# Kernel tuning notes

Hardware: AMD Instinct MI355X
Metric: run time of the kernel (lower is better)

Reference implementation:

```python
import jax, jax.numpy as jnp
import numpy as np

NH = 8        # num_heads
HD = 6        # head_dim
DIM = NH * HD # 48
KS = 3        # kernel_size
NT = KS ** 3  # 27 neighborhood tokens
SCALE = HD ** -0.5


def setup_inputs() -> dict:
    key = jax.random.key(0)
    k1, k2, k3 = jax.random.split(key, 3)
    B, H, W, T = 1, 40, 40, 40
    q = jax.random.normal(k1, (B, H, W, T, DIM), jnp.float32)
    k = jax.random.normal(k2, (B, H, W, T, DIM), jnp.float32)
    # learned relative position bias (torch init is zeros; use small noise so it matters)
    rpb = jax.random.normal(k3, (NH, KS, KS, KS), jnp.float32) * 0.02
    return {"q": q, "k": k, "rpb": rpb}


def _neighborhood_attention(q, k, rpb):
    B, H, W, T, C = q.shape
    # pad keys by win_size=1 on each spatial side (zero pad, as in nnf.pad)
    kp = jnp.pad(k, ((0, 0), (1, 1), (1, 1), (1, 1), (0, 0)))
    # gather the 27 shifted views -> [B,H,W,T,27,C] (equivalent of unfold+permute)
    win = jnp.stack(
        [kp[:, i:i + H, j:j + W, l:l + T, :]
         for i in range(KS) for j in range(KS) for l in range(KS)],
        axis=4,
    )
    qh = q.reshape(B, H, W, T, NH, HD) * SCALE          # [B,H,W,T,nh,hd]
    kh = win.reshape(B, H, W, T, NT, NH, HD)            # [B,H,W,T,27,nh,hd]
    attn = jnp.einsum('bxyzhd,bxyzkhd->bxyzhk', qh, kh)
    attn = attn + rpb.reshape(NH, NT)[None, None, None, None]  # rel-pos bias
    attn = jax.nn.softmax(attn, axis=-1)                # [B,H,W,T,nh,27]
    # value = constant integer offsets of the 3x3x3 window (makeV)
    r = jnp.arange(-(KS // 2), KS // 2 + 1, dtype=q.dtype)
    offs = jnp.stack(jnp.meshgrid(r, r, r, indexing='ij'), axis=-1).reshape(NT, 3)
    out = jnp.einsum('bxyzhk,ko->bxyzho', attn, offs)   # [B,H,W,T,nh,3]
    return out.reshape(B, H, W, T, NH * 3).transpose(0, 4, 1, 2, 3)


def reference(q, k, rpb):
    return _neighborhood_attention(q, k, rpb)
```

## Files before the change

### kernel.cpp

```cpp
#include <hip/hip_runtime.h>


#define GS   40
#define NVOX (GS*GS*GS)
#define VST  36

typedef __fp16 half2_t __attribute__((ext_vector_type(2)));
typedef float  f2      __attribute__((ext_vector_type(2)));

__device__ __forceinline__ float fdot2(half2_t a, half2_t b, float c) {
    return __builtin_amdgcn_fdot2(a, b, c, false);
}
__device__ __forceinline__ half2_t h2(unsigned int u) {
    return __builtin_bit_cast(half2_t, u);
}
__device__ __forceinline__ unsigned int pk(float a, float b) {
    return __builtin_bit_cast(unsigned int, __builtin_amdgcn_cvt_pkrtz(a, b));
}

__global__ __launch_bounds__(512, 4) void natt_kernel(
    const float* __restrict__ q, const float* __restrict__ kk,
    const float* __restrict__ rpb, float* __restrict__ out)
{
    __shared__ __align__(16) unsigned int sk[360 * VST];
    __shared__ float srpb[4 * 72];

    int t = threadIdx.x;
    int b = blockIdx.x;
    int xcd = b & 7, off = b >> 3;
    int w = (xcd < 4 ? xcd * 63 : 252 + (xcd - 4) * 62) + off;
    int bz = w % 5, byx = w / 5;
    int by = byx % 10, bx = byx / 10;
    int x0 = bx * 4, y0 = by * 4, z0 = bz * 8;

    int hp = t & 3;
    int v  = t >> 2;
    int vz = v & 7, vy = (v >> 3) & 3, vx = v >> 5;
    int gvox = (x0 + vx) * 1600 + (y0 + vy) * 40 + (z0 + vz);
    const float4* qp = (const float4*)q + (size_t)gvox * 12 + hp * 3;
    float4 qa = qp[0], qb = qp[1], qc = qp[2];

    if (t < 216) {
        int h = t / 27, n = t - h * 27;
        int i = n / 9, r9 = n - i * 9;
        int j = r9 / 3, l = r9 - j * 3;
        srpb[(h >> 1) * 72 + ((i * 3 + j) * 4 + l) * 2 + (h & 1)] =
            rpb[t] * 1.4426950408889634f;
    }

    if (t < 360) {
        int hx = t / 60, r60 = t - hx * 60;
        int hy = r60 / 10, hz = r60 - hy * 10;
        int gx = x0 + hx - 1, gy = y0 + hy - 1, gz = z0 + hz - 1;
        unsigned m = (((unsigned)gx < GS) & ((unsigned)gy < GS) &
                      ((unsigned)gz < GS)) ? 0xffffffffu : 0u;
        int cx = min(max(gx, 0), GS - 1);
        int cy = min(max(gy, 0), GS - 1);
        int cz = min(max(gz, 0), GS - 1);
        const float4* src = (const float4*)kk +
                            (size_t)(cx * 1600 + cy * 40 + cz) * 12;
        unsigned int* dst = sk + t * VST;
        #pragma unroll
        for (int hpc = 0; hpc < 4; ++hpc) {
            float4 f0 = src[hpc * 3 + 0];
            float4 f1 = src[hpc * 3 + 1];
            float4 fv = src[hpc * 3 + 2];
            uint4 u4v;
            u4v.x = pk(f0.x, f0.y) & m; u4v.y = pk(f0.z, f0.w) & m;
            u4v.z = pk(f1.x, f1.y) & m; u4v.w = pk(f1.z, f1.w) & m;
            uint2 u2v;
            u2v.x = pk(fv.x, fv.y) & m; u2v.y = pk(fv.z, fv.w) & m;
            *(uint4*)(dst + hpc * 8)     = u4v;
            *(uint2*)(dst + hpc * 8 + 4) = u2v;
        }
    }

    const float QS = 0.4082482904638631f * 1.4426950408889634f;
    half2_t qh0 = __builtin_amdgcn_cvt_pkrtz(qa.x*QS, qa.y*QS);
    half2_t qh1 = __builtin_amdgcn_cvt_pkrtz(qa.z*QS, qa.w*QS);
    half2_t qh2 = __builtin_amdgcn_cvt_pkrtz(qb.x*QS, qb.y*QS);
    half2_t qh3 = __builtin_amdgcn_cvt_pkrtz(qb.z*QS, qb.w*QS);
    half2_t qh4 = __builtin_amdgcn_cvt_pkrtz(qc.x*QS, qc.y*QS);
    half2_t qh5 = __builtin_amdgcn_cvt_pkrtz(qc.z*QS, qc.w*QS);

    __syncthreads();

    const unsigned int* kbp = sk + ((vx * 6 + vy) * 10 + vz) * VST + hp * 8;
    const float* rbp = srpb + hp * 72;

    f2 ozc = {0,0};
    f2 xb0 = {0,0}, xb1 = {0,0}, xb2 = {0,0};
    f2 yb0 = {0,0}, yb1 = {0,0}, yb2 = {0,0};

    #pragma unroll
    for (int i = 0; i < 3; ++i)
    #pragma unroll
    for (int j = 0; j < 3; ++j) {
        const unsigned int* cb = kbp + (i * 60 + j * 10) * VST;
        float4 rp01 = *(const float4*)(rbp + (i * 3 + j) * 8);
        f2     rp2v = *(const f2*)(rbp + (i * 3 + j) * 8 + 4);
        f2 ev[3];
        #pragma unroll
        for (int l = 0; l < 3; ++l) {
            uint4 a = *(const uint4*)(cb + l * VST);
            uint2 c = *(const uint2*)(cb + l * VST + 4);
            float rx = (l == 0) ? rp01.x : (l == 1) ? rp01.z : rp2v.x;
            float ry = (l == 0) ? rp01.y : (l == 1) ? rp01.w : rp2v.y;
            float d0 = fdot2(qh0, h2(a.x),
                       fdot2(qh1, h2(a.y),
                       fdot2(qh2, h2(a.z), rx)));
            float d1 = fdot2(qh3, h2(a.w),
                       fdot2(qh4, h2(c.x),
                       fdot2(qh5, h2(c.y), ry)));
            ev[l].x = __builtin_amdgcn_exp2f(d0);
            ev[l].y = __builtin_amdgcn_exp2f(d1);
        }
        f2 A = ev[0] + ev[1] + ev[2];
        ozc += ev[2] - ev[0];
        if (i == 0)      xb0 += A;
        else if (i == 1) xb1 += A;
        else             xb2 += A;
        if (j == 0)      yb0 += A;
        else if (j == 1) yb1 += A;
        else             yb2 += A;
    }

    f2 den = xb0 + xb1 + xb2;
    f2 oxv = xb2 - xb0, oyv = yb2 - yb0;
    float inv0 = __builtin_amdgcn_rcpf(den.x);
    float inv1 = __builtin_amdgcn_rcpf(den.y);

    float* op = out + (size_t)(hp * 6) * NVOX + gvox;
    op[0*NVOX] = oxv.x * inv0;
    op[1*NVOX] = oyv.x * inv0;
    op[2*NVOX] = ozc.x * inv0;
    op[3*NVOX] = oxv.y * inv1;
    op[4*NVOX] = oyv.y * inv1;
    op[5*NVOX] = ozc.y * inv1;
}

extern "C" void kernel_launch(void* const* d_in, const int* in_sizes, int n_in,
                              void* d_out, int out_size, void* d_ws, size_t ws_size,
                              hipStream_t stream) {
    const float* q   = (const float*)d_in[0];
    const float* k   = (const float*)d_in[1];
    const float* rpb = (const float*)d_in[2];
    float* out = (float*)d_out;

    natt_kernel<<<500, 512, 0, stream>>>(q, k, rpb, out);
}
```

Baseline: 13.78 us.

## Add interior fast path for K halo load, packed math, and wave priority

Adds a block-uniform interior check so blocks whose halo lies fully inside the grid load all 12 float4s without clamping or masking. Issuing all loads before packing is meant to improve memory-level parallelism. Rewrites the q scaling and output normalization as packed 2-wide float multiplies, and raises wave priority with s_setprio around the compute loop. The main cost is higher register pressure from holding 12 float4s, under launch bounds of 512 threads and 4 blocks.

Result: faster. 13.31 us (-3.4%).

```diff
diff --git a/kernel.cpp b/kernel.cpp
--- a/kernel.cpp
+++ b/kernel.cpp
@@ -48,23 +48,37 @@
             rpb[t] * 1.4426950408889634f;
     }
 
+    bool interior = (x0 >= 1) & (x0 <= 35) & (y0 >= 1) & (y0 <= 35) &
+                    (z0 >= 1) & (z0 <= 31);
     if (t < 360) {
         int hx = t / 60, r60 = t - hx * 60;
         int hy = r60 / 10, hz = r60 - hy * 10;
         int gx = x0 + hx - 1, gy = y0 + hy - 1, gz = z0 + hz - 1;
-        unsigned m = (((unsigned)gx < GS) & ((unsigned)gy < GS) &
-                      ((unsigned)gz < GS)) ? 0xffffffffu : 0u;
-        int cx = min(max(gx, 0), GS - 1);
-        int cy = min(max(gy, 0), GS - 1);
-        int cz = min(max(gz, 0), GS - 1);
-        const float4* src = (const float4*)kk +
-                            (size_t)(cx * 1600 + cy * 40 + cz) * 12;
         unsigned int* dst = sk + t * VST;
+        float4 f[12];
+        unsigned m;
+        if (interior) {
+            const float4* src = (const float4*)kk +
+                                (size_t)(gx * 1600 + gy * 40 + gz) * 12;
+            #pragma unroll
+            for (int g = 0; g < 12; ++g) f[g] = src[g];
+            m = 0xffffffffu;
+        } else {
+            m = (((unsigned)gx < GS) & ((unsigned)gy < GS) &
+                 ((unsigned)gz < GS)) ? 0xffffffffu : 0u;
+            int cx = min(max(gx, 0), GS - 1);
+            int cy = min(max(gy, 0), GS - 1);
+            int cz = min(max(gz, 0), GS - 1);
+            const float4* src = (const float4*)kk +
+                                (size_t)(cx * 1600 + cy * 40 + cz) * 12;
+            #pragma unroll
+            for (int g = 0; g < 12; ++g) f[g] = src[g];
+        }
         #pragma unroll
         for (int hpc = 0; hpc < 4; ++hpc) {
-            float4 f0 = src[hpc * 3 + 0];
-            float4 f1 = src[hpc * 3 + 1];
-            float4 fv = src[hpc * 3 + 2];
+            float4 f0 = f[hpc * 3 + 0];
+            float4 f1 = f[hpc * 3 + 1];
+            float4 fv = f[hpc * 3 + 2];
             uint4 u4v;
             u4v.x = pk(f0.x, f0.y) & m; u4v.y = pk(f0.z, f0.w) & m;
             u4v.z = pk(f1.x, f1.y) & m; u4v.w = pk(f1.z, f1.w) & m;
@@ -76,15 +90,20 @@
     }
 
     const float QS = 0.4082482904638631f * 1.4426950408889634f;
-    half2_t qh0 = __builtin_amdgcn_cvt_pkrtz(qa.x*QS, qa.y*QS);
-    half2_t qh1 = __builtin_amdgcn_cvt_pkrtz(qa.z*QS, qa.w*QS);
-    half2_t qh2 = __builtin_amdgcn_cvt_pkrtz(qb.x*QS, qb.y*QS);
-    half2_t qh3 = __builtin_amdgcn_cvt_pkrtz(qb.z*QS, qb.w*QS);
-    half2_t qh4 = __builtin_amdgcn_cvt_pkrtz(qc.x*QS, qc.y*QS);
-    half2_t qh5 = __builtin_amdgcn_cvt_pkrtz(qc.z*QS, qc.w*QS);
+    const f2 QS2 = {QS, QS};
+    f2 p0 = f2{qa.x, qa.y} * QS2, p1 = f2{qa.z, qa.w} * QS2;
+    f2 p2 = f2{qb.x, qb.y} * QS2, p3 = f2{qb.z, qb.w} * QS2;
+    f2 p4 = f2{qc.x, qc.y} * QS2, p5 = f2{qc.z, qc.w} * QS2;
+    half2_t qh0 = __builtin_amdgcn_cvt_pkrtz(p0.x, p0.y);
+    half2_t qh1 = __builtin_amdgcn_cvt_pkrtz(p1.x, p1.y);
+    half2_t qh2 = __builtin_amdgcn_cvt_pkrtz(p2.x, p2.y);
+    half2_t qh3 = __builtin_amdgcn_cvt_pkrtz(p3.x, p3.y);
+    half2_t qh4 = __builtin_amdgcn_cvt_pkrtz(p4.x, p4.y);
+    half2_t qh5 = __builtin_amdgcn_cvt_pkrtz(p5.x, p5.y);
 
     __syncthreads();
 
+    __builtin_amdgcn_s_setprio(1);
     const unsigned int* kbp = sk + ((vx * 6 + vy) * 10 + vz) * VST + hp * 8;
     const float* rbp = srpb + hp * 72;
 
@@ -124,19 +143,22 @@
         else if (j == 1) yb1 += A;
         else             yb2 += A;
     }
+    __builtin_amdgcn_s_setprio(0);
 
     f2 den = xb0 + xb1 + xb2;
     f2 oxv = xb2 - xb0, oyv = yb2 - yb0;
-    float inv0 = __builtin_amdgcn_rcpf(den.x);
-    float inv1 = __builtin_amdgcn_rcpf(den.y);
+    f2 invv;
+    invv.x = __builtin_amdgcn_rcpf(den.x);
+    invv.y = __builtin_amdgcn_rcpf(den.y);
+    f2 oxs = oxv * invv, oys = oyv * invv, ozs = ozc * invv;
 
     float* op = out + (size_t)(hp * 6) * NVOX + gvox;
-    op[0*NVOX] = oxv.x * inv0;
-    op[1*NVOX] = oyv.x * inv0;
-    op[2*NVOX] = ozc.x * inv0;
-    op[3*NVOX] = oxv.y * inv1;
-    op[4*NVOX] = oyv.y * inv1;
-    op[5*NVOX] = ozc.y * inv1;
+    op[0*NVOX] = oxs.x;
+    op[1*NVOX] = oys.x;
+    op[2*NVOX] = ozs.x;
+    op[3*NVOX] = oxs.y;
+    op[4*NVOX] = oys.y;
+    op[5*NVOX] = ozs.y;
 }
 
 extern "C" void kernel_launch(void* const* d_in, const int* in_sizes, int n_in,
```
